# Kernel optimization log

Measured on AMD Instinct MI355X. Metric: run time of the kernel, lower is better.

The kernel has to match this reference:

```python
import jax, jax.numpy as jnp
import numpy as np

N = 200000
X_SIZE = 256
H_SIZE = 256


def setup_inputs() -> dict:
    key = jax.random.key(0)
    k1, k2, k3, k4, k5 = jax.random.split(key, 5)
    x = jax.random.normal(k1, (N, X_SIZE), dtype=jnp.float32)
    Uh_sum = jax.random.normal(k2, (N, 3 * H_SIZE), dtype=jnp.float32)
    fc_sum = jax.random.normal(k3, (N, H_SIZE), dtype=jnp.float32)
    W_iou = jax.random.normal(k4, (3 * H_SIZE, X_SIZE), dtype=jnp.float32) * (X_SIZE ** -0.5)
    b_iou = jnp.zeros((1, 3 * H_SIZE), dtype=jnp.float32)
    W_f = jax.random.normal(k5, (H_SIZE, X_SIZE), dtype=jnp.float32) * (X_SIZE ** -0.5)
    b_f = jnp.zeros((1, H_SIZE), dtype=jnp.float32)
    return {"x": x, "Uh_sum": Uh_sum, "fc_sum": fc_sum,
            "W_iou": W_iou, "b_iou": b_iou, "W_f": W_f, "b_f": b_f}


def reference(x, Uh_sum, fc_sum, W_iou, b_iou, W_f, b_f):
    # init_matrices: per-node input projections
    x_iou = jnp.einsum('nd,kd->nk', x, W_iou) + b_iou   # [N, 3H]
    x_f = jnp.einsum('nd,kd->nk', x, W_f) + b_f         # [N, H]
    # apply_node_func: fused gate update with aggregated child messages
    iou = x_iou + Uh_sum
    i, o, u = jnp.split(iou, 3, axis=1)
    c = jax.nn.sigmoid(i) * jnp.tanh(u) + fc_sum
    h = jax.nn.sigmoid(o) * jnp.tanh(c)
    return h, c, x_f
```

## Files before the change

### kernel.cpp

```cpp
#include <hip/hip_runtime.h>
#include <hip/hip_bf16.h>
#include <stdint.h>


typedef __attribute__((ext_vector_type(8))) short bf16x8;
typedef __attribute__((ext_vector_type(4))) float f4v;

#define N_ROWS 200000
#define TILES 12500
#define XSTR 258
#define VMW(N) asm volatile("s_waitcnt vmcnt(" #N ")" ::: "memory")
#define SBR() __builtin_amdgcn_sched_barrier(0)

__device__ __forceinline__ bf16x8 pack8(f4v a, f4v b) {
    union { __hip_bfloat162 h2[4]; bf16x8 v; } u;
    u.h2[0] = __float22bfloat162_rn(make_float2(a.x, a.y));
    u.h2[1] = __float22bfloat162_rn(make_float2(a.z, a.w));
    u.h2[2] = __float22bfloat162_rn(make_float2(b.x, b.y));
    u.h2[3] = __float22bfloat162_rn(make_float2(b.z, b.w));
    return u.v;
}
__device__ __forceinline__ float fsig(float x) { return 1.0f / (1.0f + __expf(-x)); }
__device__ __forceinline__ float ftanh(float x) {
    float e = __expf(2.0f * x);
    return 1.0f - 2.0f / (e + 1.0f);
}

__global__ __launch_bounds__(512)
__attribute__((amdgpu_waves_per_eu(2, 2)))
void treelstm_main(const float* __restrict__ x,
                   const float* __restrict__ Uh,
                   const float* __restrict__ fc,
                   const float* __restrict__ W_iou,
                   const float* __restrict__ b_iou,
                   const float* __restrict__ W_f,
                   const float* __restrict__ b_f,
                   float* __restrict__ out) {
    __shared__ float xlds[4][16 * XSTR];

    const int tid   = threadIdx.x;
    const int lane  = tid & 63;
    const int w     = tid >> 6;
    const int q     = lane >> 4;
    const int bcol  = lane & 15;
    const int half  = blockIdx.x >> 7;
    const int phase = blockIdx.x & 127;
    const int sl    = half * 8 + w;
    const int kb    = sl * 16 + q * 4;
    const int C     = sl * 16 + bcol;

    const f4v bI = *(const f4v*)&b_iou[kb];
    const f4v bO = *(const f4v*)&b_iou[256 + kb];
    const f4v bU = *(const f4v*)&b_iou[512 + kb];
    const f4v bF = *(const f4v*)&b_f[kb];

    bf16x8 wreg[32];
#pragma unroll
    for (int g = 0; g < 4; ++g) {
        const float* wr = (g < 3) ? (W_iou + (size_t)(g * 256 + C) * 256)
                                  : (W_f + (size_t)C * 256);
#pragma unroll
        for (int ks = 0; ks < 8; ++ks) {
            const f4v p0 = *(const f4v*)(wr + ks * 32 + q * 8);
            const f4v p1 = *(const f4v*)(wr + ks * 32 + q * 8 + 4);
            wreg[g * 8 + ks] = pack8(p0, p1);
        }
    }
    VMW(0); SBR();

    float* out_h = out;
    float* out_c = out + (size_t)N_ROWS * 256;
    float* out_f = out + 2 * (size_t)N_ROWS * 256;

    const int cnt   = (TILES - phase + 127) >> 7;
    const int pairs = cnt >> 1;
    const int tail  = cnt & 1;

    auto TN = [&](int j) { const int jj = (j < cnt) ? j : (cnt - 1);
                           return phase + (jj << 7); };

    auto STAGE = [&](int t, int rb) {
#pragma unroll
        for (int rr = 0; rr < 2; ++rr) {
            const int r = 2 * w + rr;
            const float* src = x + (size_t)(t * 16 + r) * 256 + lane * 4;
            __builtin_amdgcn_global_load_lds(
                (const __attribute__((address_space(1))) uint32_t*)src,
                (__attribute__((address_space(3))) uint32_t*)&xlds[rb][r * XSTR],
                16, 0, 0);
        }
        SBR();
    };

    auto LOADUH = [&](int t, f4v& ui, f4v& uo, f4v& uu, f4v& fv) {
        const float* uh = Uh + (size_t)(t * 16 + bcol) * 768 + kb;
        ui = __builtin_nontemporal_load((const f4v*)uh);
        uo = __builtin_nontemporal_load((const f4v*)(uh + 256));
        uu = __builtin_nontemporal_load((const f4v*)(uh + 512));
        fv = __builtin_nontemporal_load((const f4v*)(fc + (size_t)(t * 16 + bcol) * 256 + kb));
    };

    auto WORK = [&](int rb, int t, const f4v& ui, const f4v& uo,
                    const f4v& uu, const f4v& fv) {
        f4v a0 = bI, a1 = bO, a2 = bU, a3 = bF;
#pragma unroll
        for (int ks = 0; ks < 8; ++ks) {
            const f4v p0 = *(const f4v*)&xlds[rb][bcol * XSTR + ks * 32 + q * 8];
            const f4v p1 = *(const f4v*)&xlds[rb][bcol * XSTR + ks * 32 + q * 8 + 4];
            const bf16x8 xf = pack8(p0, p1);
            a0 = __builtin_amdgcn_mfma_f32_16x16x32_bf16(wreg[0 * 8 + ks], xf, a0, 0, 0, 0);
            a1 = __builtin_amdgcn_mfma_f32_16x16x32_bf16(wreg[1 * 8 + ks], xf, a1, 0, 0, 0);
            a2 = __builtin_amdgcn_mfma_f32_16x16x32_bf16(wreg[2 * 8 + ks], xf, a2, 0, 0, 0);
            a3 = __builtin_amdgcn_mfma_f32_16x16x32_bf16(wreg[3 * 8 + ks], xf, a3, 0, 0, 0);
        }
        const int n = t * 16 + bcol;
        f4v cc, hh, ff;
        cc.x = fsig(a0.x + ui.x) * ftanh(a2.x + uu.x) + fv.x;
        cc.y = fsig(a0.y + ui.y) * ftanh(a2.y + uu.y) + fv.y;
        cc.z = fsig(a0.z + ui.z) * ftanh(a2.z + uu.z) + fv.z;
        cc.w = fsig(a0.w + ui.w) * ftanh(a2.w + uu.w) + fv.w;
        hh.x = fsig(a1.x + uo.x) * ftanh(cc.x);
        hh.y = fsig(a1.y + uo.y) * ftanh(cc.y);
        hh.z = fsig(a1.z + uo.z) * ftanh(cc.z);
        hh.w = fsig(a1.w + uo.w) * ftanh(cc.w);
        ff.x = a3.x; ff.y = a3.y; ff.z = a3.z; ff.w = a3.w;
        const size_t oidx = (size_t)n * 256 + kb;
        *(f4v*)(out_h + oidx) = hh;
        *(f4v*)(out_c + oidx) = cc;
        *(f4v*)(out_f + oidx) = ff;
    };

    f4v uhiA, uhoA, uhuA, fcvA, uhiB, uhoB, uhuB, fcvB;

    STAGE(TN(0), 0); LOADUH(TN(0), uhiA, uhoA, uhuA, fcvA);
    STAGE(TN(1), 1); LOADUH(TN(1), uhiB, uhoB, uhuB, fcvB);
    VMW(10);
    __builtin_amdgcn_s_barrier(); SBR();

    for (int i = 0; i < pairs; ++i) {
        const int j0 = 2 * i;
        const int rA = (i & 1) ? 2 : 0;
        const int rB = rA + 1;
        const int sA = (i & 1) ? 0 : 2;
        const int sB = sA + 1;

        STAGE(TN(j0 + 2), sA);
        WORK(rA, TN(j0), uhiA, uhoA, uhuA, fcvA);
        LOADUH(TN(j0 + 2), uhiA, uhoA, uhuA, fcvA);
        if (i == 0) { VMW(13); } else { VMW(16); }
        __builtin_amdgcn_s_barrier(); SBR();

        STAGE(TN(j0 + 3), sB);
        WORK(rB, TN(j0 + 1), uhiB, uhoB, uhuB, fcvB);
        LOADUH(TN(j0 + 3), uhiB, uhoB, uhuB, fcvB);
        VMW(16);
        __builtin_amdgcn_s_barrier(); SBR();
    }

    if (tail) {
        const int rA = (pairs & 1) ? 2 : 0;
        WORK(rA, TN(cnt - 1), uhiA, uhoA, uhuA, fcvA);
    }
}

extern "C" void kernel_launch(void* const* d_in, const int* in_sizes, int n_in,
                              void* d_out, int out_size, void* d_ws, size_t ws_size,
                              hipStream_t stream) {
    const float* x     = (const float*)d_in[0];
    const float* Uh    = (const float*)d_in[1];
    const float* fc    = (const float*)d_in[2];
    const float* W_iou = (const float*)d_in[3];
    const float* b_iou = (const float*)d_in[4];
    const float* W_f   = (const float*)d_in[5];
    const float* b_f   = (const float*)d_in[6];
    float* out = (float*)d_out;

    treelstm_main<<<256, 512, 0, stream>>>(x, Uh, fc, W_iou, b_iou, W_f, b_f, out);
}
```

Baseline: 362.8 us.

## Restructure pipeline to process three tiles per barrier with six LDS buffers

The x staging pipeline changes from double-buffered pairs to groups of three tiles over six LDS buffers, so there is one barrier per three tiles instead of one per tile. Uh and fc loads are no longer prefetched a stage ahead; they are issued at the start of each group, just before its compute. This removes barrier and sync overhead and deepens the x prefetch, but it exposes Uh/fc load latency inside the group and raises LDS use. The vmcnt waits were adjusted to match the new instruction counts.

New measurement: 383.2 us. 5.6% more time.

```diff
diff --git a/kernel.cpp b/kernel.cpp
--- a/kernel.cpp
+++ b/kernel.cpp
@@ -36,7 +36,7 @@
                    const float* __restrict__ W_f,
                    const float* __restrict__ b_f,
                    float* __restrict__ out) {
-    __shared__ float xlds[4][16 * XSTR];
+    __shared__ float xlds[6][16 * XSTR];
 
     const int tid   = threadIdx.x;
     const int lane  = tid & 63;
@@ -66,15 +66,14 @@
             wreg[g * 8 + ks] = pack8(p0, p1);
         }
     }
-    VMW(0); SBR();
 
     float* out_h = out;
     float* out_c = out + (size_t)N_ROWS * 256;
     float* out_f = out + 2 * (size_t)N_ROWS * 256;
 
-    const int cnt   = (TILES - phase + 127) >> 7;
-    const int pairs = cnt >> 1;
-    const int tail  = cnt & 1;
+    const int cnt = (TILES - phase + 127) >> 7;
+    const int G   = cnt / 3;
+    const int rem = cnt - 3 * G;
 
     auto TN = [&](int j) { const int jj = (j < cnt) ? j : (cnt - 1);
                            return phase + (jj << 7); };
@@ -89,7 +88,6 @@
                 (__attribute__((address_space(3))) uint32_t*)&xlds[rb][r * XSTR],
                 16, 0, 0);
         }
-        SBR();
     };
 
     auto LOADUH = [&](int t, f4v& ui, f4v& uo, f4v& uu, f4v& fv) {
@@ -130,36 +128,36 @@
         *(f4v*)(out_f + oidx) = ff;
     };
 
-    f4v uhiA, uhoA, uhuA, fcvA, uhiB, uhoB, uhuB, fcvB;
+    f4v ui0, uo0, uu0, fv0, ui1, uo1, uu1, fv1, ui2, uo2, uu2, fv2;
 
-    STAGE(TN(0), 0); LOADUH(TN(0), uhiA, uhoA, uhuA, fcvA);
-    STAGE(TN(1), 1); LOADUH(TN(1), uhiB, uhoB, uhuB, fcvB);
-    VMW(10);
+    STAGE(TN(0), 0); STAGE(TN(1), 1); STAGE(TN(2), 2);
+    VMW(0);
     __builtin_amdgcn_s_barrier(); SBR();
 
-    for (int i = 0; i < pairs; ++i) {
-        const int j0 = 2 * i;
-        const int rA = (i & 1) ? 2 : 0;
-        const int rB = rA + 1;
-        const int sA = (i & 1) ? 0 : 2;
-        const int sB = sA + 1;
+    for (int g = 0; g < G; ++g) {
+        const int j0 = 3 * g;
+        const int rB = (g & 1) * 3;
+        const int sB = 3 - rB;
 
-        STAGE(TN(j0 + 2), sA);
-        WORK(rA, TN(j0), uhiA, uhoA, uhuA, fcvA);
-        LOADUH(TN(j0 + 2), uhiA, uhoA, uhuA, fcvA);
-        if (i == 0) { VMW(13); } else { VMW(16); }
-        __builtin_amdgcn_s_barrier(); SBR();
+        LOADUH(TN(j0),     ui0, uo0, uu0, fv0);
+        LOADUH(TN(j0 + 1), ui1, uo1, uu1, fv1);
+        LOADUH(TN(j0 + 2), ui2, uo2, uu2, fv2);
+        SBR();
+        STAGE(TN(j0 + 3), sB); STAGE(TN(j0 + 4), sB + 1); STAGE(TN(j0 + 5), sB + 2);
+        SBR();
 
-        STAGE(TN(j0 + 3), sB);
-        WORK(rB, TN(j0 + 1), uhiB, uhoB, uhuB, fcvB);
-        LOADUH(TN(j0 + 3), uhiB, uhoB, uhuB, fcvB);
-        VMW(16);
+        WORK(rB,     TN(j0),     ui0, uo0, uu0, fv0);
+        WORK(rB + 1, TN(j0 + 1), ui1, uo1, uu1, fv1);
+        WORK(rB + 2, TN(j0 + 2), ui2, uo2, uu2, fv2);
+
+        VMW(9);
         __builtin_amdgcn_s_barrier(); SBR();
     }
 
-    if (tail) {
-        const int rA = (pairs & 1) ? 2 : 0;
-        WORK(rA, TN(cnt - 1), uhiA, uhoA, uhuA, fcvA);
+    const int tb = (G & 1) * 3;
+    for (int j = 0; j < rem; ++j) {
+        LOADUH(TN(3 * G + j), ui0, uo0, uu0, fv0);
+        WORK(tb + j, TN(3 * G + j), ui0, uo0, uu0, fv0);
     }
 }
 
```

## Prepack weights to bf16 and reload them per tile instead of holding in registers

Applied to the files above, without the earlier changes.

Adds a pre-pass kernel that converts W_iou and W_f to bf16 in the per-lane MFMA fragment layout and stores them in workspace. The main kernel no longer keeps 32 weight fragments resident in VGPRs for the whole run. Instead it reloads them from global memory (mostly L2 hits) on every tile, and the vmcnt waits are retuned to match. This frees registers and removes the prologue weight load, but adds 32 vector loads per tile per wave, extra memory traffic and a second kernel launch.

Measured after the change: 1.093 ms. +201.3%, slower.

```diff
diff --git a/kernel.cpp b/kernel.cpp
--- a/kernel.cpp
+++ b/kernel.cpp
@@ -26,6 +26,21 @@
     return 1.0f - 2.0f / (e + 1.0f);
 }
 
+__global__ void pack_w(const float* __restrict__ W_iou,
+                       const float* __restrict__ W_f,
+                       short* __restrict__ wpk) {
+    const int task = blockIdx.x * 256 + threadIdx.x;
+    const int l = task & 63, U = task >> 6;
+    const int ks = U & 7, g = (U >> 3) & 3, s = U >> 5;
+    const int r = l & 15, q = l >> 4;
+    const int C = s * 16 + r;
+    const float* wr = (g < 3) ? (W_iou + (size_t)(g * 256 + C) * 256)
+                              : (W_f + (size_t)C * 256);
+    const f4v* p = (const f4v*)(wr + ks * 32 + q * 8);
+    *(bf16x8*)(wpk + (size_t)task * 8) = pack8(p[0], p[1]);
+}
+
+template<bool PK>
 __global__ __launch_bounds__(512)
 __attribute__((amdgpu_waves_per_eu(2, 2)))
 void treelstm_main(const float* __restrict__ x,
@@ -35,6 +50,7 @@
                    const float* __restrict__ b_iou,
                    const float* __restrict__ W_f,
                    const float* __restrict__ b_f,
+                   const short* __restrict__ wpk,
                    float* __restrict__ out) {
     __shared__ float xlds[4][16 * XSTR];
 
@@ -49,24 +65,12 @@
     const int kb    = sl * 16 + q * 4;
     const int C     = sl * 16 + bcol;
 
+    const bf16x8* wp = (const bf16x8*)wpk;
+
     const f4v bI = *(const f4v*)&b_iou[kb];
     const f4v bO = *(const f4v*)&b_iou[256 + kb];
     const f4v bU = *(const f4v*)&b_iou[512 + kb];
     const f4v bF = *(const f4v*)&b_f[kb];
-
-    bf16x8 wreg[32];
-#pragma unroll
-    for (int g = 0; g < 4; ++g) {
-        const float* wr = (g < 3) ? (W_iou + (size_t)(g * 256 + C) * 256)
-                                  : (W_f + (size_t)C * 256);
-#pragma unroll
-        for (int ks = 0; ks < 8; ++ks) {
-            const f4v p0 = *(const f4v*)(wr + ks * 32 + q * 8);
-            const f4v p1 = *(const f4v*)(wr + ks * 32 + q * 8 + 4);
-            wreg[g * 8 + ks] = pack8(p0, p1);
-        }
-    }
-    VMW(0); SBR();
 
     float* out_h = out;
     float* out_c = out + (size_t)N_ROWS * 256;
@@ -102,16 +106,38 @@
 
     auto WORK = [&](int rb, int t, const f4v& ui, const f4v& uo,
                     const f4v& uu, const f4v& fv) {
+        bf16x8 wf[32];
+        if constexpr (PK) {
+#pragma unroll
+            for (int g = 0; g < 4; ++g)
+#pragma unroll
+                for (int ks = 0; ks < 8; ++ks)
+                    wf[g * 8 + ks] = wp[(size_t)((((sl * 4 + g) * 8) + ks)) * 64 + lane];
+        } else {
+#pragma unroll
+            for (int g = 0; g < 4; ++g) {
+                const float* wr = (g < 3) ? (W_iou + (size_t)(g * 256 + C) * 256)
+                                          : (W_f + (size_t)C * 256);
+#pragma unroll
+                for (int ks = 0; ks < 8; ++ks) {
+                    const f4v p0 = *(const f4v*)(wr + ks * 32 + q * 8);
+                    const f4v p1 = *(const f4v*)(wr + ks * 32 + q * 8 + 4);
+                    wf[g * 8 + ks] = pack8(p0, p1);
+                }
+            }
+        }
+        SBR();
+
         f4v a0 = bI, a1 = bO, a2 = bU, a3 = bF;
 #pragma unroll
         for (int ks = 0; ks < 8; ++ks) {
             const f4v p0 = *(const f4v*)&xlds[rb][bcol * XSTR + ks * 32 + q * 8];
             const f4v p1 = *(const f4v*)&xlds[rb][bcol * XSTR + ks * 32 + q * 8 + 4];
             const bf16x8 xf = pack8(p0, p1);
-            a0 = __builtin_amdgcn_mfma_f32_16x16x32_bf16(wreg[0 * 8 + ks], xf, a0, 0, 0, 0);
-            a1 = __builtin_amdgcn_mfma_f32_16x16x32_bf16(wreg[1 * 8 + ks], xf, a1, 0, 0, 0);
-            a2 = __builtin_amdgcn_mfma_f32_16x16x32_bf16(wreg[2 * 8 + ks], xf, a2, 0, 0, 0);
-            a3 = __builtin_amdgcn_mfma_f32_16x16x32_bf16(wreg[3 * 8 + ks], xf, a3, 0, 0, 0);
+            a0 = __builtin_amdgcn_mfma_f32_16x16x32_bf16(wf[0 * 8 + ks], xf, a0, 0, 0, 0);
+            a1 = __builtin_amdgcn_mfma_f32_16x16x32_bf16(wf[1 * 8 + ks], xf, a1, 0, 0, 0);
+            a2 = __builtin_amdgcn_mfma_f32_16x16x32_bf16(wf[2 * 8 + ks], xf, a2, 0, 0, 0);
+            a3 = __builtin_amdgcn_mfma_f32_16x16x32_bf16(wf[3 * 8 + ks], xf, a3, 0, 0, 0);
         }
         const int n = t * 16 + bcol;
         f4v cc, hh, ff;
@@ -147,13 +173,13 @@
         STAGE(TN(j0 + 2), sA);
         WORK(rA, TN(j0), uhiA, uhoA, uhuA, fcvA);
         LOADUH(TN(j0 + 2), uhiA, uhoA, uhuA, fcvA);
-        if (i == 0) { VMW(13); } else { VMW(16); }
+        VMW(9);
         __builtin_amdgcn_s_barrier(); SBR();
 
         STAGE(TN(j0 + 3), sB);
         WORK(rB, TN(j0 + 1), uhiB, uhoB, uhuB, fcvB);
         LOADUH(TN(j0 + 3), uhiB, uhoB, uhuB, fcvB);
-        VMW(16);
+        VMW(9);
         __builtin_amdgcn_s_barrier(); SBR();
     }
 
@@ -174,6 +200,14 @@
     const float* W_f   = (const float*)d_in[5];
     const float* b_f   = (const float*)d_in[6];
     float* out = (float*)d_out;
-
-    treelstm_main<<<256, 512, 0, stream>>>(x, Uh, fc, W_iou, b_iou, W_f, b_f, out);
-}
+    short* wpk = (short*)d_ws;
+
+    if (ws_size >= 512 * 1024) {
+        pack_w<<<128, 256, 0, stream>>>(W_iou, W_f, wpk);
+        treelstm_main<true><<<256, 512, 0, stream>>>(x, Uh, fc, W_iou, b_iou,
+                                                     W_f, b_f, wpk, out);
+    } else {
+        treelstm_main<false><<<256, 512, 0, stream>>>(x, Uh, fc, W_iou, b_iou,
+                                                      W_f, b_f, wpk, out);
+    }
+}
```
